# Optimization experiments

Measured on AMD Instinct MI355X. Metric: run time of the kernel, lower is better.

Reference implementation:

```python
import jax, jax.numpy as jnp
import numpy as np

C = 256
NUM_HEADS = 8
GROUPS = 8
EPS = 1e-5


def setup_inputs() -> dict:
    key = jax.random.key(0)
    ks = jax.random.split(key, 7)
    B, H, W = 2, 64, 64
    x = jax.random.normal(ks[0], (B, C, H, W), dtype=jnp.float32)
    gn_weight = jnp.ones((C,), dtype=jnp.float32)
    gn_bias = jnp.zeros((C,), dtype=jnp.float32)
    # 1x1 convs == per-pixel linear layers
    w_qkv = jax.random.normal(ks[1], (3 * C, C), dtype=jnp.float32) * (1.0 / np.sqrt(C))
    b_qkv = jax.random.normal(ks[2], (3 * C,), dtype=jnp.float32) * 0.01
    w_proj = jax.random.normal(ks[3], (C, C), dtype=jnp.float32) * (1.0 / np.sqrt(C))
    b_proj = jax.random.normal(ks[4], (C,), dtype=jnp.float32) * 0.01
    return {"x": x, "gn_weight": gn_weight, "gn_bias": gn_bias,
            "w_qkv": w_qkv, "b_qkv": b_qkv, "w_proj": w_proj, "b_proj": b_proj}


def reference(x, gn_weight, gn_bias, w_qkv, b_qkv, w_proj, b_proj):
    B, Cc, H, W = x.shape
    nh = NUM_HEADS
    hd = Cc // nh
    N = H * W
    scale = hd ** (-0.5)

    # GroupNorm(8, C): normalize over (C/G, H, W) per group, biased variance
    xg = x.reshape(B, GROUPS, Cc // GROUPS, H, W)
    mean = xg.mean(axis=(2, 3, 4), keepdims=True)
    var = xg.var(axis=(2, 3, 4), keepdims=True)
    hn = (xg - mean) * jax.lax.rsqrt(var + EPS)
    hn = hn.reshape(B, Cc, H, W) * gn_weight[None, :, None, None] + gn_bias[None, :, None, None]

    hf = hn.reshape(B, Cc, N)                       # [B, C, N]
    qkv = jnp.einsum('oc,bcn->bon', w_qkv, hf) + b_qkv[None, :, None]  # [B, 3C, N]
    qkv = qkv.reshape(B, 3, nh, hd, N)
    # q,k,v: [B, nh, N, hd]
    q = jnp.transpose(qkv[:, 0], (0, 1, 3, 2))
    k = jnp.transpose(qkv[:, 1], (0, 1, 3, 2))
    v = jnp.transpose(qkv[:, 2], (0, 1, 3, 2))

    attn = jnp.einsum('bhqd,bhkd->bhqk', q, k) * scale  # [B, nh, N, N]
    attn = jax.nn.softmax(attn, axis=-1)
    o = jnp.einsum('bhqk,bhkd->bhqd', attn, v)           # [B, nh, N, hd]
    o = jnp.transpose(o, (0, 1, 3, 2)).reshape(B, Cc, H, W)

    of = o.reshape(B, Cc, N)
    out = jnp.einsum('oc,bcn->bon', w_proj, of) + b_proj[None, :, None]
    return out.reshape(B, Cc, H, W)
```

## Files before the change

kernel.cpp:

```cpp
#include <hip/hip_runtime.h>


typedef _Float16 half8 __attribute__((ext_vector_type(8)));
typedef __fp16   fp16x2 __attribute__((ext_vector_type(2)));
typedef float    f32x4 __attribute__((ext_vector_type(4)));
typedef int      int2v __attribute__((ext_vector_type(2)));
typedef int      int4v __attribute__((ext_vector_type(4)));

__device__ __forceinline__ f32x4 mfma16(half8 a, half8 b, f32x4 c) {
  return __builtin_amdgcn_mfma_f32_16x16x32_f16(a, b, c, 0, 0, 0);
}

#if __has_builtin(__builtin_amdgcn_exp2f)
#define EXP2(x) __builtin_amdgcn_exp2f(x)
#else
#define EXP2(x) exp2f(x)
#endif

__device__ __forceinline__ unsigned short h_bits(_Float16 h) {
  return __builtin_bit_cast(unsigned short, h);
}
__device__ __forceinline__ int h2_bits(fp16x2 h) {
  return __builtin_bit_cast(int, h);
}

constexpr float CSCALE = (float)(1.4426950408889634 / 5.656854249492381);
constexpr float LOSC   = 2048.0f;
constexpr float ILOSC  = 1.0f / 2048.0f;

__global__ __launch_bounds__(256) void gn_stats(const float* __restrict__ x,
                                                float* __restrict__ stats) {
  const int bg = blockIdx.x, ch = blockIdx.y, tid = threadIdx.x;
  const float* p = x + (size_t)bg * 131072 + (size_t)ch * 4096;
  float s = 0.f, ss = 0.f;
#pragma unroll
  for (int j = 0; j < 4; ++j) {
    f32x4 v = *(const f32x4*)(p + j * 1024 + tid * 4);
#pragma unroll
    for (int k = 0; k < 4; ++k) { s += v[k]; ss += v[k] * v[k]; }
  }
#pragma unroll
  for (int m = 1; m <= 32; m <<= 1) { s += __shfl_xor(s, m); ss += __shfl_xor(ss, m); }
  __shared__ float red[8];
  const int wv = tid >> 6;
  if ((tid & 63) == 0) { red[wv * 2] = s; red[wv * 2 + 1] = ss; }
  __syncthreads();
  if (tid == 0) {
    float S = red[0] + red[2] + red[4] + red[6];
    float SS = red[1] + red[3] + red[5] + red[7];
    atomicAdd(&stats[bg * 2], S);
    atomicAdd(&stats[bg * 2 + 1], SS);
  }
}

__global__ __launch_bounds__(256) void gn_apply(const float* __restrict__ x,
                                                const float* __restrict__ gw,
                                                const float* __restrict__ gb,
                                                const float* __restrict__ stats,
                                                _Float16* __restrict__ hn_hi,
                                                _Float16* __restrict__ hn_lo) {
  __shared__ float tile[64 * 65];
  const int tid = threadIdx.x;
  const int a = tid & 15;
  const int row16 = tid >> 4;
  const int b = blockIdx.z, c0 = blockIdx.y * 64, n0 = blockIdx.x * 64;
#pragma unroll
  for (int m = 0; m < 4; ++m) {
    const int cl = row16 + 16 * m;
    const int c = c0 + cl;
    const int g = c >> 5;
    const float s = stats[(b * 8 + g) * 2];
    const float ss = stats[(b * 8 + g) * 2 + 1];
    const float mean = s * (1.f / 131072.f);
    const float var = ss * (1.f / 131072.f) - mean * mean;
    const float rstd = rsqrtf(var + 1e-5f);
    const float ga = gw[c] * rstd;
    const float be = gb[c] - mean * ga;
    f32x4 xv = *(const f32x4*)(x + ((size_t)(b * 256 + c)) * 4096 + n0 + a * 4);
#pragma unroll
    for (int j = 0; j < 4; ++j) tile[cl * 65 + a * 4 + j] = xv[j] * ga + be;
  }
  __syncthreads();
#pragma unroll
  for (int m = 0; m < 4; ++m) {
    const int nl = row16 + 16 * m;
    const int cb = a * 4;
    unsigned short hh[4], ll[4];
#pragma unroll
    for (int j = 0; j < 4; ++j) {
      float v = tile[(cb + j) * 65 + nl];
      _Float16 h = (_Float16)v;
      hh[j] = h_bits(h);
      ll[j] = h_bits((_Float16)((v - (float)h) * LOSC));
    }
    int2v uh, ul;
    uh[0] = hh[0] | (hh[1] << 16); uh[1] = hh[2] | (hh[3] << 16);
    ul[0] = ll[0] | (ll[1] << 16); ul[1] = ll[2] | (ll[3] << 16);
    size_t off = ((size_t)(b * 4096 + n0 + nl)) * 256 + c0 + cb;
    *(int2v*)(hn_hi + off) = uh;
    *(int2v*)(hn_lo + off) = ul;
  }
}

__global__ __launch_bounds__(256) void wsplit(const float* __restrict__ wq,
                                              const float* __restrict__ wp,
                                              _Float16* __restrict__ wqh,
                                              _Float16* __restrict__ wql,
                                              _Float16* __restrict__ wph,
                                              _Float16* __restrict__ wpl) {
  const int idx = blockIdx.x * 256 + threadIdx.x;
  if (idx < 196608) {
    float v = wq[idx];
    _Float16 h = (_Float16)v;
    wqh[idx] = h;
    wql[idx] = (_Float16)((v - (float)h) * LOSC);
  } else {
    const int i2 = idx - 196608;
    float v = wp[i2];
    _Float16 h = (_Float16)v;
    wph[i2] = h;
    wpl[i2] = (_Float16)((v - (float)h) * LOSC);
  }
}

template <int MODE>
__global__ __launch_bounds__(256) void gemm_split(
    const _Float16* __restrict__ Ahi, const _Float16* __restrict__ Alo,
    const _Float16* __restrict__ Bhi, const _Float16* __restrict__ Blo,
    const float* __restrict__ bias,
    _Float16* __restrict__ qkT, _Float16* __restrict__ v_t,
    float* __restrict__ outp) {
  __shared__ _Float16 a_lds[8192];
  __shared__ _Float16 b_lds[8192];
  const int tid = threadIdx.x, lane = tid & 63, wv = tid >> 6;
  const int qq = lane >> 4, ii = lane & 15;
  const int m0 = blockIdx.x * 64, n0 = blockIdx.y * 64, bz = blockIdx.z;
  const int hlT = (tid >> 7) & 1, cT = (tid >> 6) & 1;
  const int qT = (tid >> 4) & 3, iT = tid & 15;
  const _Float16* Asel = hlT ? Alo : Ahi;
  const _Float16* Bsel = hlT ? Blo : Bhi;
  const _Float16* aptr = Asel + (size_t)(m0 + iT) * 256 + 32 * cT + 8 * qT;
  const _Float16* bptr = Bsel + ((size_t)(bz * 4096 + n0 + iT)) * 256 + 32 * cT + 8 * qT;

  f32x4 acc[4] = {}, acc2[4] = {};
  for (int k0 = 0; k0 < 256; k0 += 64) {
#pragma unroll
    for (int j = 0; j < 4; ++j) {
      *(half8*)(a_lds + (((j * 2 + hlT) * 2 + cT) * 64 + (tid & 63)) * 8) =
          *(const half8*)(aptr + (size_t)(16 * j) * 256 + k0);
      *(half8*)(b_lds + (((j * 2 + hlT) * 2 + cT) * 64 + (tid & 63)) * 8) =
          *(const half8*)(bptr + (size_t)(16 * j) * 256 + k0);
    }
    __syncthreads();
    half8 ah[2], al[2];
#pragma unroll
    for (int c = 0; c < 2; ++c) {
      ah[c] = *(const half8*)(a_lds + (((wv * 2 + 0) * 2 + c) * 64 + lane) * 8);
      al[c] = *(const half8*)(a_lds + (((wv * 2 + 1) * 2 + c) * 64 + lane) * 8);
    }
#pragma unroll
    for (int t = 0; t < 4; ++t) {
#pragma unroll
      for (int c = 0; c < 2; ++c) {
        half8 bh_ = *(const half8*)(b_lds + (((t * 2 + 0) * 2 + c) * 64 + lane) * 8);
        half8 bl_ = *(const half8*)(b_lds + (((t * 2 + 1) * 2 + c) * 64 + lane) * 8);
        acc[t]  = mfma16(ah[c], bh_, acc[t]);
        acc2[t] = mfma16(ah[c], bl_, acc2[t]);
        acc2[t] = mfma16(al[c], bh_, acc2[t]);
      }
    }
    __syncthreads();
  }

  const int och0 = m0 + 16 * wv + 4 * qq;
  if (MODE == 0) {
    if (m0 < 512) {
      const float sc = (m0 < 256) ? CSCALE : 1.0f;
#pragma unroll
      for (int t = 0; t < 4; ++t) {
        const int n = n0 + 16 * t + ii;
        unsigned short hh[4];
#pragma unroll
        for (int r = 0; r < 4; ++r) {
          float val = (acc[t][r] + acc2[t][r] * ILOSC + bias[och0 + r]) * sc;
          hh[r] = h_bits((_Float16)val);
        }
        int2v u;
        u[0] = hh[0] | (hh[1] << 16);
        u[1] = hh[2] | (hh[3] << 16);
        *(int2v*)(qkT + ((size_t)(bz * 4096 + n)) * 512 + och0) = u;
      }
    } else {
#pragma unroll
      for (int t = 0; t < 4; ++t) {
#pragma unroll
        for (int r = 0; r < 4; ++r) {
          const int och = och0 + r;
          const int d = och - 512;
          const int hd_ = d & 31, head = d >> 5;
          const int n = n0 + 16 * t + ii;
          float val = acc[t][r] + acc2[t][r] * ILOSC + bias[och];
          v_t[((size_t)((bz * 8 + head) * 32 + hd_)) * 4096 + n] = (_Float16)val;
        }
      }
    }
  } else {
#pragma unroll
    for (int t = 0; t < 4; ++t) {
#pragma unroll
      for (int r = 0; r < 4; ++r) {
        const int och = och0 + r;
        const int n = n0 + 16 * t + ii;
        outp[((size_t)(bz * 256 + och)) * 4096 + n] =
            acc[t][r] + acc2[t][r] * ILOSC + bias[och];
      }
    }
  }
}

__global__ __launch_bounds__(256) void attn_kernel(
    const _Float16* __restrict__ qkT, const _Float16* __restrict__ v_t,
    _Float16* __restrict__ o_hi, _Float16* __restrict__ o_lo) {
  __shared__ _Float16 k_lds[2][128 * 40];
  __shared__ _Float16 v_lds[2][32 * 136];
  const int tid = threadIdx.x, lane = tid & 63, wv = tid >> 6;
  const int qq = lane >> 4, ii = lane & 15;
  const int bh = blockIdx.y, b = bh >> 3, h = bh & 7;
  const int n0 = blockIdx.x * 128;

  const _Float16* qbase =
      qkT + ((size_t)(b * 4096 + n0 + 32 * wv + ii)) * 512 + h * 32 + 8 * qq;
  half8 qf0 = *(const half8*)qbase;
  half8 qf1 = *(const half8*)(qbase + (size_t)16 * 512);

  const _Float16* ksrc[2];
  int kdst[2];
  const _Float16* vsrc[2];
  int vdst[2];
#pragma unroll
  for (int rep = 0; rep < 2; ++rep) {
    const int idx = tid + 256 * rep;
    const int slot = idx >> 2, kq = idx & 3;
    const int tau = slot >> 4, m = slot & 15;
    const int g = 32 * (tau >> 1) + 4 * (tau & 1) + 8 * (m >> 2) + (m & 3);
    ksrc[rep] = qkT + ((size_t)(b * 4096 + g)) * 512 + 256 + h * 32 + 8 * kq;
    kdst[rep] = slot * 40 + 8 * kq;
    const int d = idx >> 4, vc = idx & 15;
    vsrc[rep] = v_t + ((size_t)(bh * 32 + d)) * 4096 + 8 * vc;
    vdst[rep] = d * 136 + 8 * vc;
  }

  half8 ones8;
#pragma unroll
  for (int j = 0; j < 8; ++j) ones8[j] = (_Float16)1.0f;

  f32x4 o00 = {}, o10 = {}, o01 = {}, o11 = {}, accl0 = {}, accl1 = {};

  half8 kr0 = *(const half8*)ksrc[0];
  half8 kr1 = *(const half8*)ksrc[1];
  half8 vr0 = *(const half8*)vsrc[0];
  half8 vr1 = *(const half8*)vsrc[1];
  *(half8*)(k_lds[0] + kdst[0]) = kr0;
  *(half8*)(k_lds[0] + kdst[1]) = kr1;
  *(half8*)(v_lds[0] + vdst[0]) = vr0;
  *(half8*)(v_lds[0] + vdst[1]) = vr1;
  __syncthreads();

  for (int kb = 0; kb < 32; ++kb) {
    const int cur = kb & 1;
    if (kb < 31) {
      const size_t ko = (size_t)(kb + 1) * 128 * 512;
      const size_t vo = (size_t)(kb + 1) * 128;
      kr0 = *(const half8*)(ksrc[0] + ko);
      kr1 = *(const half8*)(ksrc[1] + ko);
      vr0 = *(const half8*)(vsrc[0] + vo);
      vr1 = *(const half8*)(vsrc[1] + vo);
    }
    const _Float16* kbase = k_lds[cur];
    const _Float16* vbase = v_lds[cur];

#pragma unroll
    for (int u = 0; u < 4; ++u) {
      half8 kfa = *(const half8*)(kbase + (32 * u + ii) * 40 + 8 * qq);
      half8 kfb = *(const half8*)(kbase + (32 * u + 16 + ii) * 40 + 8 * qq);
      f32x4 z = {};
      f32x4 sa0 = mfma16(kfa, qf0, z);
      f32x4 sb0 = mfma16(kfb, qf0, z);
      f32x4 sa1 = mfma16(kfa, qf1, z);
      f32x4 sb1 = mfma16(kfb, qf1, z);
      int4v p0, p1;
      p0[0] = h2_bits(__builtin_amdgcn_cvt_pkrtz(EXP2(sa0[0]), EXP2(sa0[1])));
      p0[1] = h2_bits(__builtin_amdgcn_cvt_pkrtz(EXP2(sa0[2]), EXP2(sa0[3])));
      p0[2] = h2_bits(__builtin_amdgcn_cvt_pkrtz(EXP2(sb0[0]), EXP2(sb0[1])));
      p0[3] = h2_bits(__builtin_amdgcn_cvt_pkrtz(EXP2(sb0[2]), EXP2(sb0[3])));
      p1[0] = h2_bits(__builtin_amdgcn_cvt_pkrtz(EXP2(sa1[0]), EXP2(sa1[1])));
      p1[1] = h2_bits(__builtin_amdgcn_cvt_pkrtz(EXP2(sa1[2]), EXP2(sa1[3])));
      p1[2] = h2_bits(__builtin_amdgcn_cvt_pkrtz(EXP2(sb1[0]), EXP2(sb1[1])));
      p1[3] = h2_bits(__builtin_amdgcn_cvt_pkrtz(EXP2(sb1[2]), EXP2(sb1[3])));
      half8 pt0 = __builtin_bit_cast(half8, p0);
      half8 pt1 = __builtin_bit_cast(half8, p1);
      half8 vf0 = *(const half8*)(vbase + ii * 136 + 32 * u + 8 * qq);
      half8 vf1 = *(const half8*)(vbase + (16 + ii) * 136 + 32 * u + 8 * qq);
      o00 = mfma16(vf0, pt0, o00);
      o10 = mfma16(vf1, pt0, o10);
      accl0 = mfma16(ones8, pt0, accl0);
      o01 = mfma16(vf0, pt1, o01);
      o11 = mfma16(vf1, pt1, o11);
      accl1 = mfma16(ones8, pt1, accl1);
    }

    if (kb < 31) {
      _Float16* kn = k_lds[cur ^ 1];
      _Float16* vn = v_lds[cur ^ 1];
      *(half8*)(kn + kdst[0]) = kr0;
      *(half8*)(kn + kdst[1]) = kr1;
      *(half8*)(vn + vdst[0]) = vr0;
      *(half8*)(vn + vdst[1]) = vr1;
    }
    __syncthreads();
  }

#pragma unroll
  for (int hf = 0; hf < 2; ++hf) {
    const f32x4& oa = hf ? o01 : o00;
    const f32x4& ob = hf ? o11 : o10;
    const float inv = 1.0f / (hf ? accl1[0] : accl0[0]);
    const size_t row =
        ((size_t)(b * 4096 + n0 + 32 * wv + 16 * hf + ii)) * 256 + h * 32;
    unsigned short hh[4], ll[4];
#pragma unroll
    for (int r = 0; r < 4; ++r) {
      float v = oa[r] * inv;
      _Float16 hv = (_Float16)v;
      hh[r] = h_bits(hv);
      ll[r] = h_bits((_Float16)((v - (float)hv) * LOSC));
    }
    int2v uh, ul;
    uh[0] = hh[0] | (hh[1] << 16); uh[1] = hh[2] | (hh[3] << 16);
    ul[0] = ll[0] | (ll[1] << 16); ul[1] = ll[2] | (ll[3] << 16);
    *(int2v*)(o_hi + row + 4 * qq) = uh;
    *(int2v*)(o_lo + row + 4 * qq) = ul;
#pragma unroll
    for (int r = 0; r < 4; ++r) {
      float v = ob[r] * inv;
      _Float16 hv = (_Float16)v;
      hh[r] = h_bits(hv);
      ll[r] = h_bits((_Float16)((v - (float)hv) * LOSC));
    }
    uh[0] = hh[0] | (hh[1] << 16); uh[1] = hh[2] | (hh[3] << 16);
    ul[0] = ll[0] | (ll[1] << 16); ul[1] = ll[2] | (ll[3] << 16);
    *(int2v*)(o_hi + row + 16 + 4 * qq) = uh;
    *(int2v*)(o_lo + row + 16 + 4 * qq) = ul;
  }
}

extern "C" void kernel_launch(void* const* d_in, const int* in_sizes, int n_in,
                              void* d_out, int out_size, void* d_ws, size_t ws_size,
                              hipStream_t stream) {
  const float* x     = (const float*)d_in[0];
  const float* gnw   = (const float*)d_in[1];
  const float* gnb   = (const float*)d_in[2];
  const float* wqkv  = (const float*)d_in[3];
  const float* bqkv  = (const float*)d_in[4];
  const float* wproj = (const float*)d_in[5];
  const float* bproj = (const float*)d_in[6];
  float* out = (float*)d_out;

  char* ws = (char*)d_ws;
  size_t off = 0;
  auto alloc = [&](size_t bytes) -> char* {
    char* p = ws + off;
    off += (bytes + 255) & ~(size_t)255;
    return p;
  };
  float*    stats  = (float*)alloc(128);
  _Float16* hn_hi  = (_Float16*)alloc((size_t)2 * 4096 * 256 * 2);
  _Float16* hn_lo  = (_Float16*)alloc((size_t)2 * 4096 * 256 * 2);
  _Float16* wq_hi  = (_Float16*)alloc((size_t)768 * 256 * 2);
  _Float16* wq_lo  = (_Float16*)alloc((size_t)768 * 256 * 2);
  _Float16* wp_hi  = (_Float16*)alloc((size_t)256 * 256 * 2);
  _Float16* wp_lo  = (_Float16*)alloc((size_t)256 * 256 * 2);
  _Float16* qkT    = (_Float16*)alloc((size_t)2 * 4096 * 512 * 2);
  _Float16* v_t    = (_Float16*)alloc((size_t)16 * 32 * 4096 * 2);
  _Float16* o_hi   = (_Float16*)alloc((size_t)2 * 4096 * 256 * 2);
  _Float16* o_lo   = (_Float16*)alloc((size_t)2 * 4096 * 256 * 2);
  if (off > ws_size) return;

  (void)hipMemsetAsync(stats, 0, 256, stream);
  gn_stats<<<dim3(16, 32), 256, 0, stream>>>(x, stats);
  gn_apply<<<dim3(64, 4, 2), 256, 0, stream>>>(x, gnw, gnb, stats, hn_hi, hn_lo);
  wsplit<<<1024, 256, 0, stream>>>(wqkv, wproj, wq_hi, wq_lo, wp_hi, wp_lo);
  gemm_split<0><<<dim3(12, 64, 2), 256, 0, stream>>>(wq_hi, wq_lo, hn_hi, hn_lo,
                                                     bqkv, qkT, v_t, nullptr);
  attn_kernel<<<dim3(32, 16), 256, 0, stream>>>(qkT, v_t, o_hi, o_lo);
  gemm_split<1><<<dim3(4, 64, 2), 256, 0, stream>>>(wp_hi, wp_lo, o_hi, o_lo,
                                                    bproj, nullptr, nullptr, out);
}
```

Before: 179.0 us.

## Split attention keys into two partitions with a combine kernel

```diff
diff --git a/kernel.cpp b/kernel.cpp
--- a/kernel.cpp
+++ b/kernel.cpp
@@ -220,13 +220,15 @@
 
 __global__ __launch_bounds__(256) void attn_kernel(
     const _Float16* __restrict__ qkT, const _Float16* __restrict__ v_t,
-    _Float16* __restrict__ o_hi, _Float16* __restrict__ o_lo) {
-  __shared__ _Float16 k_lds[2][128 * 40];
-  __shared__ _Float16 v_lds[2][32 * 136];
+    float* __restrict__ opart, float* __restrict__ lpart) {
+  __shared__ _Float16 k_lds[2][4096];
+  __shared__ _Float16 v_lds[2][4096];
   const int tid = threadIdx.x, lane = tid & 63, wv = tid >> 6;
   const int qq = lane >> 4, ii = lane & 15;
   const int bh = blockIdx.y, b = bh >> 3, h = bh & 7;
   const int n0 = blockIdx.x * 128;
+  const int part = blockIdx.z;
+  const int key0 = part * 2048;
 
   const _Float16* qbase =
       qkT + ((size_t)(b * 4096 + n0 + 32 * wv + ii)) * 512 + h * 32 + 8 * qq;
@@ -234,20 +236,18 @@
   half8 qf1 = *(const half8*)(qbase + (size_t)16 * 512);
 
   const _Float16* ksrc[2];
-  int kdst[2];
   const _Float16* vsrc[2];
-  int vdst[2];
+  int dst8[2];
 #pragma unroll
   for (int rep = 0; rep < 2; ++rep) {
     const int idx = tid + 256 * rep;
-    const int slot = idx >> 2, kq = idx & 3;
-    const int tau = slot >> 4, m = slot & 15;
-    const int g = 32 * (tau >> 1) + 4 * (tau & 1) + 8 * (m >> 2) + (m & 3);
-    ksrc[rep] = qkT + ((size_t)(b * 4096 + g)) * 512 + 256 + h * 32 + 8 * kq;
-    kdst[rep] = slot * 40 + 8 * kq;
-    const int d = idx >> 4, vc = idx & 15;
-    vsrc[rep] = v_t + ((size_t)(bh * 32 + d)) * 4096 + 8 * vc;
-    vdst[rep] = d * 136 + 8 * vc;
+    dst8[rep] = idx * 8;
+    const int f = idx >> 6, l = idx & 63;
+    const int fq = l >> 4, fi = l & 15;
+    const int u = f >> 1, hf = f & 1;
+    const int g = 32 * u + 4 * hf + 8 * (fi >> 2) + (fi & 3);
+    ksrc[rep] = qkT + ((size_t)(b * 4096 + key0 + g)) * 512 + 256 + h * 32 + 8 * fq;
+    vsrc[rep] = v_t + ((size_t)(bh * 32 + 16 * hf + fi)) * 4096 + key0 + 32 * u + 8 * fq;
   }
 
   half8 ones8;
@@ -260,15 +260,15 @@
   half8 kr1 = *(const half8*)ksrc[1];
   half8 vr0 = *(const half8*)vsrc[0];
   half8 vr1 = *(const half8*)vsrc[1];
-  *(half8*)(k_lds[0] + kdst[0]) = kr0;
-  *(half8*)(k_lds[0] + kdst[1]) = kr1;
-  *(half8*)(v_lds[0] + vdst[0]) = vr0;
-  *(half8*)(v_lds[0] + vdst[1]) = vr1;
+  *(half8*)(k_lds[0] + dst8[0]) = kr0;
+  *(half8*)(k_lds[0] + dst8[1]) = kr1;
+  *(half8*)(v_lds[0] + dst8[0]) = vr0;
+  *(half8*)(v_lds[0] + dst8[1]) = vr1;
   __syncthreads();
 
-  for (int kb = 0; kb < 32; ++kb) {
+  for (int kb = 0; kb < 16; ++kb) {
     const int cur = kb & 1;
-    if (kb < 31) {
+    if (kb < 15) {
       const size_t ko = (size_t)(kb + 1) * 128 * 512;
       const size_t vo = (size_t)(kb + 1) * 128;
       kr0 = *(const half8*)(ksrc[0] + ko);
@@ -281,8 +281,8 @@
 
 #pragma unroll
     for (int u = 0; u < 4; ++u) {
-      half8 kfa = *(const half8*)(kbase + (32 * u + ii) * 40 + 8 * qq);
-      half8 kfb = *(const half8*)(kbase + (32 * u + 16 + ii) * 40 + 8 * qq);
+      half8 kfa = *(const half8*)(kbase + u * 1024 + lane * 8);
+      half8 kfb = *(const half8*)(kbase + u * 1024 + 512 + lane * 8);
       f32x4 z = {};
       f32x4 sa0 = mfma16(kfa, qf0, z);
       f32x4 sb0 = mfma16(kfb, qf0, z);
@@ -299,8 +299,8 @@
       p1[3] = h2_bits(__builtin_amdgcn_cvt_pkrtz(EXP2(sb1[2]), EXP2(sb1[3])));
       half8 pt0 = __builtin_bit_cast(half8, p0);
       half8 pt1 = __builtin_bit_cast(half8, p1);
-      half8 vf0 = *(const half8*)(vbase + ii * 136 + 32 * u + 8 * qq);
-      half8 vf1 = *(const half8*)(vbase + (16 + ii) * 136 + 32 * u + 8 * qq);
+      half8 vf0 = *(const half8*)(vbase + u * 1024 + lane * 8);
+      half8 vf1 = *(const half8*)(vbase + u * 1024 + 512 + lane * 8);
       o00 = mfma16(vf0, pt0, o00);
       o10 = mfma16(vf1, pt0, o10);
       accl0 = mfma16(ones8, pt0, accl0);
@@ -309,48 +309,50 @@
       accl1 = mfma16(ones8, pt1, accl1);
     }
 
-    if (kb < 31) {
+    if (kb < 15) {
       _Float16* kn = k_lds[cur ^ 1];
       _Float16* vn = v_lds[cur ^ 1];
-      *(half8*)(kn + kdst[0]) = kr0;
-      *(half8*)(kn + kdst[1]) = kr1;
-      *(half8*)(vn + vdst[0]) = vr0;
-      *(half8*)(vn + vdst[1]) = vr1;
+      *(half8*)(kn + dst8[0]) = kr0;
+      *(half8*)(kn + dst8[1]) = kr1;
+      *(half8*)(vn + dst8[0]) = vr0;
+      *(half8*)(vn + dst8[1]) = vr1;
     }
     __syncthreads();
   }
 
 #pragma unroll
   for (int hf = 0; hf < 2; ++hf) {
-    const f32x4& oa = hf ? o01 : o00;
-    const f32x4& ob = hf ? o11 : o10;
-    const float inv = 1.0f / (hf ? accl1[0] : accl0[0]);
-    const size_t row =
-        ((size_t)(b * 4096 + n0 + 32 * wv + 16 * hf + ii)) * 256 + h * 32;
-    unsigned short hh[4], ll[4];
-#pragma unroll
-    for (int r = 0; r < 4; ++r) {
-      float v = oa[r] * inv;
-      _Float16 hv = (_Float16)v;
-      hh[r] = h_bits(hv);
-      ll[r] = h_bits((_Float16)((v - (float)hv) * LOSC));
-    }
-    int2v uh, ul;
-    uh[0] = hh[0] | (hh[1] << 16); uh[1] = hh[2] | (hh[3] << 16);
-    ul[0] = ll[0] | (ll[1] << 16); ul[1] = ll[2] | (ll[3] << 16);
-    *(int2v*)(o_hi + row + 4 * qq) = uh;
-    *(int2v*)(o_lo + row + 4 * qq) = ul;
-#pragma unroll
-    for (int r = 0; r < 4; ++r) {
-      float v = ob[r] * inv;
-      _Float16 hv = (_Float16)v;
-      hh[r] = h_bits(hv);
-      ll[r] = h_bits((_Float16)((v - (float)hv) * LOSC));
-    }
-    uh[0] = hh[0] | (hh[1] << 16); uh[1] = hh[2] | (hh[3] << 16);
-    ul[0] = ll[0] | (ll[1] << 16); ul[1] = ll[2] | (ll[3] << 16);
-    *(int2v*)(o_hi + row + 16 + 4 * qq) = uh;
-    *(int2v*)(o_lo + row + 16 + 4 * qq) = ul;
+    const f32x4 oa = hf ? o01 : o00;
+    const f32x4 ob = hf ? o11 : o10;
+    const int q = n0 + 32 * wv + 16 * hf + ii;
+    float* base = opart + ((size_t)((part * 2 + b) * 4096 + q)) * 256 + h * 32;
+    *(f32x4*)(base + 4 * qq) = oa;
+    *(f32x4*)(base + 16 + 4 * qq) = ob;
+    if (qq == 0) {
+      lpart[((size_t)((part * 2 + b) * 4096 + q)) * 8 + h] = hf ? accl1[0] : accl0[0];
+    }
+  }
+}
+
+__global__ __launch_bounds__(256) void attn_combine(
+    const float* __restrict__ opart, const float* __restrict__ lpart,
+    _Float16* __restrict__ o_hi, _Float16* __restrict__ o_lo) {
+  const int c = threadIdx.x, hh = c >> 5;
+#pragma unroll
+  for (int k = 0; k < 4; ++k) {
+    const int row = blockIdx.x * 4 + k;
+    const int b = row >> 12;
+    const size_t i0 = ((size_t)(0 * 2 + b) * 4096 + (row & 4095)) * 256 + c;
+    const size_t i1 = ((size_t)(1 * 2 + b) * 4096 + (row & 4095)) * 256 + c;
+    const size_t l0i = ((size_t)(0 * 2 + b) * 4096 + (row & 4095)) * 8 + hh;
+    const size_t l1i = ((size_t)(1 * 2 + b) * 4096 + (row & 4095)) * 8 + hh;
+    const float O = opart[i0] + opart[i1];
+    const float inv = 1.0f / (lpart[l0i] + lpart[l1i]);
+    const float v = O * inv;
+    _Float16 hv = (_Float16)v;
+    const size_t out = (size_t)row * 256 + c;
+    o_hi[out] = hv;
+    o_lo[out] = (_Float16)((v - (float)hv) * LOSC);
   }
 }
 
@@ -382,8 +384,10 @@
   _Float16* wp_lo  = (_Float16*)alloc((size_t)256 * 256 * 2);
   _Float16* qkT    = (_Float16*)alloc((size_t)2 * 4096 * 512 * 2);
   _Float16* v_t    = (_Float16*)alloc((size_t)16 * 32 * 4096 * 2);
-  _Float16* o_hi   = (_Float16*)alloc((size_t)2 * 4096 * 256 * 2);
-  _Float16* o_lo   = (_Float16*)alloc((size_t)2 * 4096 * 256 * 2);
+  float*    opart  = (float*)alloc((size_t)4 * 4096 * 256 * 4);
+  float*    lpart  = (float*)alloc((size_t)4 * 4096 * 8 * 4);
+  _Float16* o_hi = hn_hi;
+  _Float16* o_lo = hn_lo;
   if (off > ws_size) return;
 
   (void)hipMemsetAsync(stats, 0, 256, stream);
@@ -392,7 +396,8 @@
   wsplit<<<1024, 256, 0, stream>>>(wqkv, wproj, wq_hi, wq_lo, wp_hi, wp_lo);
   gemm_split<0><<<dim3(12, 64, 2), 256, 0, stream>>>(wq_hi, wq_lo, hn_hi, hn_lo,
                                                      bqkv, qkT, v_t, nullptr);
-  attn_kernel<<<dim3(32, 16), 256, 0, stream>>>(qkT, v_t, o_hi, o_lo);
+  attn_kernel<<<dim3(32, 16, 2), 256, 0, stream>>>(qkT, v_t, opart, lpart);
+  attn_combine<<<2048, 256, 0, stream>>>(opart, lpart, o_hi, o_lo);
   gemm_split<1><<<dim3(4, 64, 2), 256, 0, stream>>>(wp_hi, wp_lo, o_hi, o_lo,
                                                     bproj, nullptr, nullptr, out);
 }
```

Result: no change. 178.2 us (-0.4%).
